# Optimization experiments

Measured on AMD Instinct MI355X. Metric: run time of the kernel, lower is better.

## Reference

```python
import jax, jax.numpy as jnp
import numpy as np

B, C, H, W = 32, 384, 32, 32
NCH = 4           # chunks per branch (mixing_size = [4,4,4])
CH = C // NCH     # 96 channels per chunk


def setup_inputs() -> dict:
    key = jax.random.key(0)
    ks = iter(jax.random.split(key, 32))
    r = lambda shape, s=0.05: jax.random.normal(next(ks), shape, dtype=jnp.float32) * s
    inp = {"x": jax.random.normal(next(ks), (B, C, H, W), dtype=jnp.float32)}
    for b, k in zip((1, 2, 3), (1, 3, 5)):
        inp[f"f{b}_mlp_w1"] = r((2, CH, CH // 8))
        inp[f"f{b}_mlp_b1"] = r((2, CH // 8))
        inp[f"f{b}_mlp_w2"] = r((2, CH // 8, CH))
        inp[f"f{b}_mlp_b2"] = r((2, CH))
        inp[f"f{b}_conv_w"] = r((2, CH, 1, k, k))
        inp[f"f{b}_conv_b"] = r((2, CH))
    inp["fusion_w1"] = r((C, C // 4))
    inp["fusion_b1"] = r((C // 4,))
    inp["fusion_w2"] = r((C // 4, 3 * C))
    inp["fusion_b2"] = r((3 * C,))
    inp["proj_w"] = r((C, C))
    inp["proj_b"] = r((C,))
    return inp


def _gelu(x):
    return jax.nn.gelu(x, approximate=False)  # torch nn.GELU default (erf)


def _branch(x, mw1, mb1, mw2, mb2, cw, cb, pad):
    # x: (B, C, H, W); chunks of CH channels; even idx -> MLP (channel-last), odd -> depthwise conv
    chunks = jnp.split(x, NCH, axis=1)
    outs, mi, ci = [], 0, 0
    for i, c in enumerate(chunks):
        if i % 2 == 0:
            h = _gelu(jnp.einsum('bchw,cd->bdhw', c, mw1[mi]) + mb1[mi][:, None, None])
            y = jnp.einsum('bdhw,dc->bchw', h, mw2[mi]) + mb2[mi][:, None, None]
            mi += 1
        else:
            y = jax.lax.conv_general_dilated(
                c, cw[ci], window_strides=(1, 1), padding=[(pad, pad), (pad, pad)],
                feature_group_count=CH, dimension_numbers=('NCHW', 'OIHW', 'NCHW'))
            y = y + cb[ci][:, None, None]
            ci += 1
        outs.append(y)
    return jnp.concatenate(outs, axis=1)


def reference(x,
              f1_mlp_w1, f1_mlp_b1, f1_mlp_w2, f1_mlp_b2, f1_conv_w, f1_conv_b,
              f2_mlp_w1, f2_mlp_b1, f2_mlp_w2, f2_mlp_b2, f2_conv_w, f2_conv_b,
              f3_mlp_w1, f3_mlp_b1, f3_mlp_w2, f3_mlp_b2, f3_conv_w, f3_conv_b,
              fusion_w1, fusion_b1, fusion_w2, fusion_b2, proj_w, proj_b):
    x1 = _branch(x, f1_mlp_w1, f1_mlp_b1, f1_mlp_w2, f1_mlp_b2, f1_conv_w, f1_conv_b, pad=0)
    x2 = _branch(x, f2_mlp_w1, f2_mlp_b1, f2_mlp_w2, f2_mlp_b2, f2_conv_w, f2_conv_b, pad=1)
    x3 = _branch(x, f3_mlp_w1, f3_mlp_b1, f3_mlp_w2, f3_mlp_b2, f3_conv_w, f3_conv_b, pad=2)
    # softmax-gated multi-scale fusion
    a = (x1 + x2 + x3).mean(axis=(2, 3))                            # (B, C)
    g = _gelu(a @ fusion_w1 + fusion_b1) @ fusion_w2 + fusion_b2     # (B, 3C)
    g = g.reshape(a.shape[0], C, 3).transpose(2, 0, 1)               # (3, B, C)
    w = jax.nn.softmax(g, axis=0)[:, :, :, None, None]               # (3, B, C, 1, 1)
    comb = x1 * w[0] + x2 * w[1] + x3 * w[2]                         # (B, C, H, W)
    out = jnp.einsum('bchw,cd->bdhw', comb, proj_w) + proj_b[:, None, None]
    return out
```

## Files before the change

### kernel.cpp

```cpp
#include <hip/hip_runtime.h>
#include <math.h>

#define B_  32
#define C_  384
#define HW  1024

typedef float          f32x4 __attribute__((ext_vector_type(4)));
typedef short          s16x8 __attribute__((ext_vector_type(8)));
typedef unsigned short us8v  __attribute__((ext_vector_type(8)));

#define SWZ(pix) ((((pix) ^ ((pix) >> 4)) & 15) << 4)

struct KParams {
  const float* x;
  const float* mw1[3]; const float* mb1[3]; const float* mw2[3]; const float* mb2[3];
  const float* cw[3];  const float* cb[3];
  const float* fw1; const float* fb1; const float* fw2; const float* fb2;
  const float* pw;  const float* pb;
  float* wg;
  float* H_part;
  float* cvA;
  float* ext;
  unsigned short* pwT;
  float* out;
};

__device__ __forceinline__ float gelu_exact(float v) {
  return 0.5f * v * (1.0f + erff(v * 0.70710678118654752440f));
}
__device__ __forceinline__ unsigned short f2bf(float f) {
  unsigned u = __float_as_uint(f);
  u += 0x7FFFu + ((u >> 16) & 1u);
  return (unsigned short)(u >> 16);
}
__device__ __forceinline__ float bf2f(unsigned short h) {
  return __uint_as_float(((unsigned)h) << 16);
}

template<int HALF>
__device__ __forceinline__ void conv_strip(const float* xc, int h0, int row,
                                           float w1t, const float* w3, const float* w5,
                                           float* y0, float* y1, float* y2) {
#pragma unroll
  for (int p = 0; p < 16; ++p) { y0[p] = 0.f; y1[p] = 0.f; y2[p] = 0.f; }
#pragma unroll
  for (int dy = 0; dy < 5; ++dy) {
    const int hr = h0 + row - 2 + dy;
    float win[20];
    if (hr >= 0 && hr < 32) {
#pragma unroll
      for (int u = 0; u < 5; ++u)
        *(float4*)&win[u*4] = *(const float4*)&xc[hr*32 + HALF*12 + u*4];
    } else {
#pragma unroll
      for (int u = 0; u < 20; ++u) win[u] = 0.f;
    }
#pragma unroll
    for (int dx = 0; dx < 5; ++dx) {
      const float w = w5[dy*5 + dx];
#pragma unroll
      for (int p = 0; p < 16; ++p) {
        const int ri = p + dx - 2 + HALF*4;
        if (ri >= 0 && ri < 20) y2[p] += win[ri] * w;
      }
    }
    if (dy >= 1 && dy <= 3) {
#pragma unroll
      for (int dx = 0; dx < 3; ++dx) {
        const float w = w3[(dy-1)*3 + dx];
#pragma unroll
        for (int p = 0; p < 16; ++p) {
          const int ri = p + dx - 1 + HALF*4;
          if (ri >= 0 && ri < 20) y1[p] += win[ri] * w;
        }
      }
      if (dy == 2) {
#pragma unroll
        for (int p = 0; p < 16; ++p) y0[p] = win[p + HALF*4] * w1t;
      }
    }
  }
}

__global__ __launch_bounds__(256, 2) void k_work(KParams P) {
  __shared__ __align__(16) char sm[49152 + 13824 + 256];
  const int bid = blockIdx.x;
  const int t = threadIdx.x;

  if (bid >= 1024) {
    const int pbk = bid - 1024;
    float (*tile)[33] = (float(*)[33])sm;
    const int td = pbk % 12, tc = pbk / 12;
    const int j = t & 31, i0 = t >> 5;
    const int gcoff = (tc < 3) ? 0 : (tc < 6 ? 96 : (tc < 9 ? -96 : 0));
    for (int i = i0; i < 32; i += 8)
      tile[i][j] = P.pw[(size_t)(tc*32 + i + gcoff)*C_ + td*32 + j];
    __syncthreads();
    for (int i = i0; i < 32; i += 8)
      P.pwT[(size_t)(td*32 + i)*C_ + tc*32 + j] = f2bf(tile[j][i]);
    return;
  }

  const int b = bid >> 5, sub = bid & 31;
  if (sub < 16) {
    const int mi = sub >> 3, q = sub & 7;
    const int h0 = q * 4;
    float* Xl  = (float*)sm;
    float* w1l = (float*)(sm + 49152);
    float* Hl  = (float*)(sm + 49152 + 13824);
    for (int i = t; i < 3456; i += 256) {
      int s = i / 1152, r = i - s*1152;
      w1l[i] = P.mw1[s][mi*1152 + r];
    }
    for (int i = t*4; i < 12288; i += 1024) {
      int c = i >> 7, pix = i & 127;
      *(float4*)&Xl[i] = *(const float4*)&P.x[(size_t)(b*C_ + mi*192 + c)*HW + h0*32 + pix];
    }
    __syncthreads();
    const int quad = t & 31, sjg = t >> 6;
    const int cq = (t >> 5) & 1;
    const int sj0 = sjg * 9;
    float h[9][4];
#pragma unroll
    for (int u = 0; u < 9; ++u) { h[u][0]=0.f; h[u][1]=0.f; h[u][2]=0.f; h[u][3]=0.f; }
    int wbase[9];
#pragma unroll
    for (int u = 0; u < 9; ++u) {
      int sj = sj0 + u, s = sj / 12, jj = sj % 12;
      wbase[u] = s*1152 + jj;
    }
    for (int c = cq*48; c < cq*48 + 48; ++c) {
      const float4 xv = *(const float4*)&Xl[c*128 + quad*4];
#pragma unroll
      for (int u = 0; u < 9; ++u) {
        const float w = w1l[wbase[u] + c*12];
        h[u][0] += xv.x*w; h[u][1] += xv.y*w; h[u][2] += xv.z*w; h[u][3] += xv.w*w;
      }
    }
#pragma unroll
    for (int u = 0; u < 9; ++u)
#pragma unroll
      for (int p = 0; p < 4; ++p) h[u][p] += __shfl_xor(h[u][p], 32, 64);
    float hs[9];
#pragma unroll
    for (int u = 0; u < 9; ++u) {
      int sj = sj0 + u, s = sj / 12, jj = sj % 12;
      const float bias = P.mb1[s][mi*12 + jj];
      float sum = 0.f;
#pragma unroll
      for (int p = 0; p < 4; ++p) sum += gelu_exact(h[u][p] + bias);
#pragma unroll
      for (int m = 16; m >= 1; m >>= 1) sum += __shfl_xor(sum, m, 64);
      hs[u] = sum;
    }
    if ((t & 63) == 0) {
#pragma unroll
      for (int u = 0; u < 9; ++u) Hl[sj0 + u] = hs[u];
    }
    __syncthreads();
    if (t < 36) P.H_part[(size_t)((b*2 + mi)*8 + q)*36 + t] = Hl[t];
  } else {
    const int s2 = sub - 16;
    const int gi = s2 >> 3, q = s2 & 7;
    const int h0 = q * 4;
    const int lane = t & 63, wv = t >> 6;
    const int gcbase = (2*gi + 1) * 96;
    for (int i = 0; i < 24; ++i) {
      const int cc = wv*24 + i;
      const float* xc = P.x + (size_t)(b*C_ + gcbase + cc)*HW + h0*32;
      const float2 v = *(const float2*)(xc + 2*lane);
      const float t2 = v.x + v.y;
      float T = t2;
      T += __shfl_xor(T, 1, 64);  T += __shfl_xor(T, 2, 64);
      T += __shfl_xor(T, 4, 64);  T += __shfl_xor(T, 8, 64);
      T += __shfl_xor(T, 16, 64); T += __shfl_xor(T, 32, 64);
      float c0  = ((lane & 15) == 0)  ? v.x : 0.f;
      float c1  = ((lane & 15) == 0)  ? v.y : 0.f;
      float c30 = ((lane & 15) == 15) ? v.x : 0.f;
      float c31 = ((lane & 15) == 15) ? v.y : 0.f;
      c0  += __shfl_xor(c0, 16, 64);  c0  += __shfl_xor(c0, 32, 64);
      c1  += __shfl_xor(c1, 16, 64);  c1  += __shfl_xor(c1, 32, 64);
      c30 += __shfl_xor(c30, 16, 64); c30 += __shfl_xor(c30, 32, 64);
      c31 += __shfl_xor(c31, 16, 64); c31 += __shfl_xor(c31, 32, 64);
      if (lane == 0) {
        float* A = &P.cvA[(size_t)(b*2 + gi)*5*96 + cc];
        atomicAdd(A + 0*96, T);   atomicAdd(A + 1*96, c0);
        atomicAdd(A + 2*96, c1);  atomicAdd(A + 3*96, c30);
        atomicAdd(A + 4*96, c31);
      }
      if (q == 0 || q == 7) {
        float r = t2;
        r += __shfl_xor(r, 1, 64); r += __shfl_xor(r, 2, 64);
        r += __shfl_xor(r, 4, 64); r += __shfl_xor(r, 8, 64);
        const int e  = (q == 0) ? 0 : 1;
        const int lo = (q == 0) ? 0 : 32;
        const float Ra  = __shfl(r,   lo,      64), Rb  = __shfl(r,   lo + 16, 64);
        const float p00 = __shfl(v.x, lo,      64), p01 = __shfl(v.y, lo,      64);
        const float p0a = __shfl(v.x, lo + 15, 64), p0b = __shfl(v.y, lo + 15, 64);
        const float p10 = __shfl(v.x, lo + 16, 64), p11 = __shfl(v.y, lo + 16, 64);
        const float p1a = __shfl(v.x, lo + 31, 64), p1b = __shfl(v.y, lo + 31, 64);
        if (lane == 0) {
          float* E = &P.ext[((size_t)(b*2 + gi)*2 + e)*10*96 + cc];
          E[0*96] = Ra;  E[1*96] = Rb;
          E[2*96] = p00; E[3*96] = p01; E[4*96] = p0a; E[5*96] = p0b;
          E[6*96] = p10; E[7*96] = p11; E[8*96] = p1a; E[9*96] = p1b;
        }
      }
    }
  }
}

__global__ __launch_bounds__(512) void k_gate(KParams P) {
  const int b = blockIdx.x, t = threadIdx.x;
  __shared__ float am[C_], g1p[4][96], g1v[96], Hs[2][36];
  for (int i = t; i < 72; i += 512) {
    int mi = i / 36, sj = i % 36;
    float s = 0.f;
    for (int q = 0; q < 8; ++q) s += P.H_part[(size_t)((b*2+mi)*8 + q)*36 + sj];
    Hs[mi][sj] = s * (1.0f/1024.0f);
  }
  __syncthreads();
  if (t < 192) {
    const int mi = t / 96, cc = t % 96;
    float a = 0.f;
    for (int s = 0; s < 3; ++s) {
      float y = P.mb2[s][mi*96 + cc];
      for (int jj = 0; jj < 12; ++jj) y += Hs[mi][s*12+jj] * P.mw2[s][mi*1152 + jj*96 + cc];
      a += y;
    }
    am[mi*192 + cc] = a;
  } else if (t < 384) {
    const int i = t - 192;
    const int gi = i / 96, cc = i % 96;
    const float* A  = &P.cvA[(size_t)(b*2 + gi)*5*96 + cc];
    const float T   = A[0*96];
    const float C0  = A[1*96], C1  = A[2*96], C30 = A[3*96], C31 = A[4*96];
    const float* E0 = &P.ext[((size_t)(b*2 + gi)*2 + 0)*10*96 + cc];
    const float* E1 = &P.ext[((size_t)(b*2 + gi)*2 + 1)*10*96 + cc];
    const float R0  = E0[0*96], R1  = E0[1*96];
    const float a00 = E0[2*96], a01 = E0[3*96], a0a = E0[4*96], a0b = E0[5*96];
    const float a10 = E0[6*96], a11 = E0[7*96], a1a = E0[8*96], a1b = E0[9*96];
    const float R30 = E1[0*96], R31 = E1[1*96];
    const float b00 = E1[2*96], b01 = E1[3*96], b0a = E1[4*96], b0b = E1[5*96];
    const float b10 = E1[6*96], b11 = E1[7*96], b1a = E1[8*96], b1b = E1[9*96];
    const float ER[5]   = {R30+R31, R31, 0.f, R0, R0+R1};
    const float EC[5]   = {C30+C31, C31, 0.f, C0, C0+C1};
    const float cr0[5]  = {a0a+a0b, a0b, 0.f, a00, a00+a01};
    const float cr1[5]  = {a1a+a1b, a1b, 0.f, a10, a10+a11};
    const float cr30[5] = {b0a+b0b, b0b, 0.f, b00, b00+b01};
    const float cr31[5] = {b1a+b1b, b1b, 0.f, b10, b10+b11};
    const int gcl = gi*96 + cc;
    float sum = P.cw[0][gcl] * T;
#pragma unroll
    for (int dy = 0; dy < 3; ++dy)
#pragma unroll
      for (int dx = 0; dx < 3; ++dx) {
        const int s = dy - 1, u = dx - 1;
        float xc_ = 0.f;
        if (s == 1)  xc_ = cr0[u+2];
        if (s == -1) xc_ = cr31[u+2];
        sum += P.cw[1][gcl*9 + dy*3 + dx] * (T - ER[s+2] - EC[u+2] + xc_);
      }
#pragma unroll
    for (int dy = 0; dy < 5; ++dy)
#pragma unroll
      for (int dx = 0; dx < 5; ++dx) {
        const int s = dy - 2, u = dx - 2;
        float xc_ = 0.f;
        if (s == 1)  xc_ = cr0[u+2];
        if (s == 2)  xc_ = cr0[u+2] + cr1[u+2];
        if (s == -1) xc_ = cr31[u+2];
        if (s == -2) xc_ = cr30[u+2] + cr31[u+2];
        sum += P.cw[2][gcl*25 + dy*5 + dx] * (T - ER[s+2] - EC[u+2] + xc_);
      }
    am[(2*gi+1)*96 + cc] = sum * (1.0f/1024.0f)
                         + P.cb[0][gcl] + P.cb[1][gcl] + P.cb[2][gcl];
  }
  __syncthreads();
  if (t < 384) {
    const int quarter = t / 96, jj = t % 96;
    float acc = 0.f;
    for (int c = quarter*96; c < quarter*96 + 96; ++c) acc += am[c] * P.fw1[c*96 + jj];
    g1p[quarter][jj] = acc;
  }
  __syncthreads();
  if (t < 96) g1v[t] = gelu_exact(g1p[0][t] + g1p[1][t] + g1p[2][t] + g1p[3][t] + P.fb1[t]);
  __syncthreads();
  if (t < 384) {
    const int c = t;
    float l0 = P.fb2[c*3+0], l1 = P.fb2[c*3+1], l2 = P.fb2[c*3+2];
    for (int jj = 0; jj < 96; ++jj) {
      const float g = g1v[jj];
      const float* f = P.fw2 + jj*1152 + c*3;
      l0 += g*f[0]; l1 += g*f[1]; l2 += g*f[2];
    }
    const float m = fmaxf(l0, fmaxf(l1, l2));
    const float e0 = expf(l0-m), e1 = expf(l1-m), e2 = expf(l2-m);
    const float inv = 1.0f/(e0+e1+e2);
    P.wg[0*(B_*C_) + b*C_ + c] = e0*inv;
    P.wg[1*(B_*C_) + b*C_ + c] = e1*inv;
    P.wg[2*(B_*C_) + b*C_ + c] = e2*inv;
  }
}

template<int HALF>
__device__ __forceinline__ void conv_phase2(const KParams& P, int b, int h0,
                                            char* combB, const float* wgl, int tt) {
  for (int it = 0; it < 2; ++it) {
    const int task = tt + 512*it;
    if (task < 768) {
      const int row = task & 3, c192 = task >> 2;
      const int gi = c192 / 96, cc = c192 - gi*96;
      const int gcl = gi*96 + cc;
      const int gc = (2*gi + 1)*96 + cc;
      const int kp = 192 + gi*96 + cc;
      const float* xc = P.x + (size_t)(b*C_ + gc)*HW;
      const float w1t = P.cw[0][gcl];
      float w3[9], w5[25];
#pragma unroll
      for (int k2 = 0; k2 < 9; ++k2)  w3[k2] = P.cw[1][gcl*9 + k2];
#pragma unroll
      for (int k2 = 0; k2 < 25; ++k2) w5[k2] = P.cw[2][gcl*25 + k2];
      float y0[16], y1[16], y2[16];
      conv_strip<HALF>(xc, h0, row, w1t, w3, w5, y0, y1, y2);
      const float g0 = wgl[0*C_ + gc], g1 = wgl[1*C_ + gc], g2 = wgl[2*C_ + gc];
      const float cbg = g0*P.cb[0][gcl] + g1*P.cb[1][gcl] + g2*P.cb[2][gcl];
#pragma unroll
      for (int p = 0; p < 16; ++p) {
        const float v = g0*y0[p] + g1*y1[p] + g2*y2[p] + cbg;
        const int pix = row*32 + HALF*16 + p;
        const int off = pix*768 + ((kp*2) ^ SWZ(pix));
        *(unsigned short*)(combB + off) = f2bf(v);
      }
    }
  }
}

__global__ __launch_bounds__(1024, 4) void k_proj(KParams P) {
  __shared__ __align__(16) char smem[159744];
  char* combB = smem;
  char* hlB   = smem + 98304;
  char* XB    = smem + 116736;
  unsigned short* wlB = (unsigned short*)(smem + 141312);
  float* wgl  = (float*)(smem + 155136);

  const int t  = threadIdx.x;
  const int rb = (blockIdx.x & 7) * 32 + (blockIdx.x >> 3);
  const int b  = rb >> 3;
  const int h0 = (rb & 7) * 4;

  for (int i = t; i < 1152; i += 1024)
    wgl[i] = P.wg[(size_t)(i/C_)*(B_*C_) + b*C_ + (i % C_)];
  for (int i = t; i < 6912; i += 1024) {
    int s = i / 2304, r = i - s*2304, mi2 = r / 1152, rr = r - mi2*1152;
    int c = rr / 12, jj = rr - c*12;
    wlB[(s*2 + mi2)*1152 + jj*96 + c] = f2bf(P.mw1[s][mi2*1152 + rr]);
  }
  for (int i = t*4; i < 12288; i += 4096) {
    int c = i >> 7, pix = i & 127;
    float4 v = *(const float4*)&P.x[(size_t)(b*C_ + c)*HW + h0*32 + pix];
    unsigned lo = (unsigned)f2bf(v.x) | ((unsigned)f2bf(v.y) << 16);
    unsigned hi = (unsigned)f2bf(v.z) | ((unsigned)f2bf(v.w) << 16);
    *(uint2*)(XB + c*256 + pix*2) = make_uint2(lo, hi);
  }
  __syncthreads();

#pragma unroll 1
  for (int mi = 0; mi < 2; ++mi) {
    if (t < 512) {
      const int w = t >> 6, l = t & 63;
      const int nsj = (w < 4) ? 5 : 4;
      const int sj0 = (w < 4) ? w*5 : 20 + (w - 4)*4;
      int wbase[5]; float bias[5];
#pragma unroll
      for (int u = 0; u < 5; ++u) {
        int sj = sj0 + ((u < nsj) ? u : 0);
        int s = sj / 12, jj = sj - s*12;
        wbase[u] = (s*2 + mi)*1152 + jj*96;
        bias[u] = P.mb1[s][mi*12 + jj];
      }
      float h[5][2];
#pragma unroll
      for (int u = 0; u < 5; ++u) { h[u][0] = 0.f; h[u][1] = 0.f; }
      for (int c0 = 0; c0 < 96; c0 += 8) {
        us8v wv8[5];
#pragma unroll
        for (int u = 0; u < 5; ++u)
          wv8[u] = *(const us8v*)(wlB + wbase[u] + c0);
#pragma unroll
        for (int cc = 0; cc < 8; ++cc) {
          const unsigned xp = *(const unsigned*)(XB + (c0 + cc)*256 + l*4);
          const float x0 = __uint_as_float(xp << 16);
          const float x1 = __uint_as_float(xp & 0xFFFF0000u);
#pragma unroll
          for (int u = 0; u < 5; ++u) {
            if (u < nsj) {
              const float wv = bf2f(wv8[u][cc]);
              h[u][0] += x0*wv; h[u][1] += x1*wv;
            }
          }
        }
      }
#pragma unroll
      for (int u = 0; u < 5; ++u) {
        if (u < nsj) {
          const unsigned o = (unsigned)f2bf(gelu_exact(h[u][0] + bias[u]))
                           | ((unsigned)f2bf(gelu_exact(h[u][1] + bias[u])) << 16);
          *(unsigned*)(hlB + (mi*36 + sj0 + u)*256 + l*4) = o;
        }
      }
    } else {
      if (mi == 0) conv_phase2<0>(P, b, h0, combB, wgl, t - 512);
      else         conv_phase2<1>(P, b, h0, combB, wgl, t - 512);
    }
    __syncthreads();
    if (mi == 0) {
      for (int i = t*4; i < 12288; i += 4096) {
        int c = i >> 7, pix = i & 127;
        float4 v = *(const float4*)&P.x[(size_t)(b*C_ + 192 + c)*HW + h0*32 + pix];
        unsigned lo = (unsigned)f2bf(v.x) | ((unsigned)f2bf(v.y) << 16);
        unsigned hi = (unsigned)f2bf(v.z) | ((unsigned)f2bf(v.w) << 16);
        *(uint2*)(XB + c*256 + pix*2) = make_uint2(lo, hi);
      }
      __syncthreads();
    }
  }

  for (int i = t; i < 6912; i += 1024) {
    int s = i / 2304, r = i - s*2304, mi2 = r / 1152, rr = r - mi2*1152;
    wlB[(s*2 + mi2)*1152 + rr] = f2bf(P.mw2[s][mi2*1152 + rr]);
  }
  __syncthreads();

  {
    const int ct = t & 31, pt = (t >> 5) & 15, mi = t >> 9;
    const int c0 = ct*3, pix0 = pt*8;
    float wgc[3][3];
#pragma unroll
    for (int s = 0; s < 3; ++s)
#pragma unroll
      for (int i = 0; i < 3; ++i) wgc[s][i] = wgl[s*C_ + mi*192 + c0 + i];
    float acc[3][8];
#pragma unroll
    for (int i = 0; i < 3; ++i) {
      float ai = 0.f;
#pragma unroll
      for (int s = 0; s < 3; ++s) ai += wgc[s][i] * P.mb2[s][mi*96 + c0 + i];
#pragma unroll
      for (int p = 0; p < 8; ++p) acc[i][p] = ai;
    }
#pragma unroll
    for (int s = 0; s < 3; ++s)
#pragma unroll
      for (int jj = 0; jj < 12; ++jj) {
        const us8v hv = *(const us8v*)(hlB + (mi*36 + s*12 + jj)*256 + pix0*2);
        float hf[8];
#pragma unroll
        for (int p = 0; p < 8; ++p) hf[p] = bf2f(hv[p]);
        const unsigned short* wp = wlB + (s*2 + mi)*1152 + jj*96 + c0;
        float gw[3];
#pragma unroll
        for (int i = 0; i < 3; ++i) gw[i] = bf2f(wp[i]) * wgc[s][i];
#pragma unroll
        for (int i = 0; i < 3; ++i)
#pragma unroll
          for (int p = 0; p < 8; ++p) acc[i][p] += gw[i]*hf[p];
      }
#pragma unroll
    for (int i = 0; i < 3; ++i)
#pragma unroll
      for (int p = 0; p < 8; ++p) {
        const int pix = pix0 + p;
        const int kp2 = mi*96 + c0 + i;
        const int off = pix*768 + ((kp2*2) ^ SWZ(pix));
        *(unsigned short*)(combB + off) = f2bf(acc[i][p]);
      }
  }
  __syncthreads();

  {
    const int lane = t & 63, wv = t >> 6;
    const int wm = wv & 1, wn = wv >> 1;
    const int l15 = lane & 15, l4 = lane >> 4;
    f32x4 acc[4][3];
#pragma unroll
    for (int mt = 0; mt < 4; ++mt)
#pragma unroll
      for (int nt = 0; nt < 3; ++nt) acc[mt][nt] = (f32x4){0.f,0.f,0.f,0.f};
    const char* pwTb = (const char*)P.pwT;
#pragma unroll 2
    for (int ks = 0; ks < 12; ++ks) {
      const int k0 = ks*32 + l4*8;
      s16x8 af[4], bfr[3];
#pragma unroll
      for (int mt = 0; mt < 4; ++mt) {
        const int m = wm*64 + mt*16 + l15;
        af[mt] = *(const s16x8*)(combB + m*768 + ((2*k0) ^ SWZ(m)));
      }
#pragma unroll
      for (int nt = 0; nt < 3; ++nt) {
        const int d = wn*48 + nt*16 + l15;
        bfr[nt] = *(const s16x8*)(pwTb + (size_t)d*768 + 2*k0);
      }
#pragma unroll
      for (int mt = 0; mt < 4; ++mt)
#pragma unroll
        for (int nt = 0; nt < 3; ++nt)
          acc[mt][nt] = __builtin_amdgcn_mfma_f32_16x16x32_bf16(af[mt], bfr[nt], acc[mt][nt], 0, 0, 0);
    }
#pragma unroll
    for (int nt = 0; nt < 3; ++nt) {
      const int d = wn*48 + nt*16 + l15;
      const float pbv = P.pb[d];
#pragma unroll
      for (int mt = 0; mt < 4; ++mt) {
        const int pix = wm*64 + mt*16 + l4*4;
        float4 o;
        o.x = acc[mt][nt][0] + pbv;
        o.y = acc[mt][nt][1] + pbv;
        o.z = acc[mt][nt][2] + pbv;
        o.w = acc[mt][nt][3] + pbv;
        *(float4*)&P.out[(size_t)(b*C_ + d)*HW + (h0 + (pix >> 5))*32 + (pix & 31)] = o;
      }
    }
  }
}

extern "C" void kernel_launch(void* const* d_in, const int* in_sizes, int n_in,
                              void* d_out, int out_size, void* d_ws, size_t ws_size,
                              hipStream_t stream) {
  KParams P;
  P.x = (const float*)d_in[0];
  for (int s = 0; s < 3; ++s) {
    const int base = 1 + s * 6;
    P.mw1[s] = (const float*)d_in[base + 0];
    P.mb1[s] = (const float*)d_in[base + 1];
    P.mw2[s] = (const float*)d_in[base + 2];
    P.mb2[s] = (const float*)d_in[base + 3];
    P.cw[s]  = (const float*)d_in[base + 4];
    P.cb[s]  = (const float*)d_in[base + 5];
  }
  P.fw1 = (const float*)d_in[19]; P.fb1 = (const float*)d_in[20];
  P.fw2 = (const float*)d_in[21]; P.fb2 = (const float*)d_in[22];
  P.pw  = (const float*)d_in[23]; P.pb  = (const float*)d_in[24];
  float* w = (float*)d_ws;
  P.wg     = w;
  P.H_part = w + 36864;
  P.cvA    = w + 55296;
  P.ext    = w + 86016;
  P.pwT    = (unsigned short*)(w + 208896);
  P.out = (float*)d_out;

  hipMemsetAsync((char*)d_ws + 55296*sizeof(float), 0, 30720*sizeof(float), stream);
  k_work<<<1168, 256, 0, stream>>>(P);
  k_gate<<<32, 512, 0, stream>>>(P);
  k_proj<<<256, 1024, 0, stream>>>(P);
}
```

Before: 289.8 us.

## Store MLP hidden activations in k_work and reuse them in k_proj

The first kernel now writes the GELU hidden activations as bf16 to a workspace buffer. The projection kernel reads them back instead of recomputing the first MLP layer, which removes the x reload and the hidden-layer recompute from k_proj. Conv partial sums are now written per strip and summed in the gate kernel rather than accumulated with atomics, so the memset can be dropped. k_proj shrinks to 512 threads with more channels per thread. The trade-off is extra global write and read traffic for the hidden buffer and lower thread-level parallelism in k_proj.

```diff
diff --git a/kernel.cpp b/kernel.cpp
--- a/kernel.cpp
+++ b/kernel.cpp
@@ -19,9 +19,10 @@
   const float* pw;  const float* pb;
   float* wg;
   float* H_part;
-  float* cvA;
+  float* cvS;
   float* ext;
   unsigned short* pwT;
+  unsigned short* hl;
   float* out;
 };
 
@@ -146,9 +147,16 @@
     for (int u = 0; u < 9; ++u) {
       int sj = sj0 + u, s = sj / 12, jj = sj % 12;
       const float bias = P.mb1[s][mi*12 + jj];
-      float sum = 0.f;
-#pragma unroll
-      for (int p = 0; p < 4; ++p) sum += gelu_exact(h[u][p] + bias);
+      float g[4];
+#pragma unroll
+      for (int p = 0; p < 4; ++p) g[p] = gelu_exact(h[u][p] + bias);
+      if ((t & 63) < 32) {
+        uint2 pk;
+        pk.x = (unsigned)f2bf(g[0]) | ((unsigned)f2bf(g[1]) << 16);
+        pk.y = (unsigned)f2bf(g[2]) | ((unsigned)f2bf(g[3]) << 16);
+        *(uint2*)(P.hl + ((size_t)(b*2 + mi)*36 + sj)*1024 + q*128 + quad*4) = pk;
+      }
+      float sum = g[0] + g[1] + g[2] + g[3];
 #pragma unroll
       for (int m = 16; m >= 1; m >>= 1) sum += __shfl_xor(sum, m, 64);
       hs[u] = sum;
@@ -183,10 +191,9 @@
       c30 += __shfl_xor(c30, 16, 64); c30 += __shfl_xor(c30, 32, 64);
       c31 += __shfl_xor(c31, 16, 64); c31 += __shfl_xor(c31, 32, 64);
       if (lane == 0) {
-        float* A = &P.cvA[(size_t)(b*2 + gi)*5*96 + cc];
-        atomicAdd(A + 0*96, T);   atomicAdd(A + 1*96, c0);
-        atomicAdd(A + 2*96, c1);  atomicAdd(A + 3*96, c30);
-        atomicAdd(A + 4*96, c31);
+        float* S = &P.cvS[(((size_t)(b*2 + gi)*8 + q)*5)*96 + cc];
+        S[0*96] = T;   S[1*96] = c0;  S[2*96] = c1;
+        S[3*96] = c30; S[4*96] = c31;
       }
       if (q == 0 || q == 7) {
         float r = t2;
@@ -232,9 +239,13 @@
   } else if (t < 384) {
     const int i = t - 192;
     const int gi = i / 96, cc = i % 96;
-    const float* A  = &P.cvA[(size_t)(b*2 + gi)*5*96 + cc];
-    const float T   = A[0*96];
-    const float C0  = A[1*96], C1  = A[2*96], C30 = A[3*96], C31 = A[4*96];
+    const float* S0 = &P.cvS[(((size_t)(b*2 + gi)*8)*5)*96 + cc];
+    float T = 0.f, C0 = 0.f, C1 = 0.f, C30 = 0.f, C31 = 0.f;
+#pragma unroll
+    for (int q = 0; q < 8; ++q) {
+      const float* Sq = S0 + (size_t)q*5*96;
+      T += Sq[0*96]; C0 += Sq[1*96]; C1 += Sq[2*96]; C30 += Sq[3*96]; C31 += Sq[4*96];
+    }
     const float* E0 = &P.ext[((size_t)(b*2 + gi)*2 + 0)*10*96 + cc];
     const float* E1 = &P.ext[((size_t)(b*2 + gi)*2 + 1)*10*96 + cc];
     const float R0  = E0[0*96], R1  = E0[1*96];
@@ -303,146 +314,73 @@
   }
 }
 
-template<int HALF>
-__device__ __forceinline__ void conv_phase2(const KParams& P, int b, int h0,
-                                            char* combB, const float* wgl, int tt) {
-  for (int it = 0; it < 2; ++it) {
-    const int task = tt + 512*it;
-    if (task < 768) {
-      const int row = task & 3, c192 = task >> 2;
-      const int gi = c192 / 96, cc = c192 - gi*96;
-      const int gcl = gi*96 + cc;
-      const int gc = (2*gi + 1)*96 + cc;
-      const int kp = 192 + gi*96 + cc;
-      const float* xc = P.x + (size_t)(b*C_ + gc)*HW;
-      const float w1t = P.cw[0][gcl];
-      float w3[9], w5[25];
-#pragma unroll
-      for (int k2 = 0; k2 < 9; ++k2)  w3[k2] = P.cw[1][gcl*9 + k2];
-#pragma unroll
-      for (int k2 = 0; k2 < 25; ++k2) w5[k2] = P.cw[2][gcl*25 + k2];
-      float y0[16], y1[16], y2[16];
-      conv_strip<HALF>(xc, h0, row, w1t, w3, w5, y0, y1, y2);
-      const float g0 = wgl[0*C_ + gc], g1 = wgl[1*C_ + gc], g2 = wgl[2*C_ + gc];
-      const float cbg = g0*P.cb[0][gcl] + g1*P.cb[1][gcl] + g2*P.cb[2][gcl];
-#pragma unroll
-      for (int p = 0; p < 16; ++p) {
-        const float v = g0*y0[p] + g1*y1[p] + g2*y2[p] + cbg;
-        const int pix = row*32 + HALF*16 + p;
-        const int off = pix*768 + ((kp*2) ^ SWZ(pix));
-        *(unsigned short*)(combB + off) = f2bf(v);
-      }
-    }
-  }
-}
-
-__global__ __launch_bounds__(1024, 4) void k_proj(KParams P) {
-  __shared__ __align__(16) char smem[159744];
+__global__ __launch_bounds__(512, 1) void k_proj(KParams P) {
+  __shared__ __align__(16) char smem[135168];
   char* combB = smem;
   char* hlB   = smem + 98304;
-  char* XB    = smem + 116736;
-  unsigned short* wlB = (unsigned short*)(smem + 141312);
-  float* wgl  = (float*)(smem + 155136);
+  unsigned short* wlB = (unsigned short*)(smem + 117120);
+  float* wgl  = (float*)(smem + 130944);
 
   const int t  = threadIdx.x;
   const int rb = (blockIdx.x & 7) * 32 + (blockIdx.x >> 3);
   const int b  = rb >> 3;
-  const int h0 = (rb & 7) * 4;
-
-  for (int i = t; i < 1152; i += 1024)
+  const int qv = rb & 7;
+  const int h0 = qv * 4;
+
+  for (int i = t; i < 1152; i += 512)
     wgl[i] = P.wg[(size_t)(i/C_)*(B_*C_) + b*C_ + (i % C_)];
-  for (int i = t; i < 6912; i += 1024) {
-    int s = i / 2304, r = i - s*2304, mi2 = r / 1152, rr = r - mi2*1152;
-    int c = rr / 12, jj = rr - c*12;
-    wlB[(s*2 + mi2)*1152 + jj*96 + c] = f2bf(P.mw1[s][mi2*1152 + rr]);
-  }
-  for (int i = t*4; i < 12288; i += 4096) {
-    int c = i >> 7, pix = i & 127;
-    float4 v = *(const float4*)&P.x[(size_t)(b*C_ + c)*HW + h0*32 + pix];
-    unsigned lo = (unsigned)f2bf(v.x) | ((unsigned)f2bf(v.y) << 16);
-    unsigned hi = (unsigned)f2bf(v.z) | ((unsigned)f2bf(v.w) << 16);
-    *(uint2*)(XB + c*256 + pix*2) = make_uint2(lo, hi);
-  }
-  __syncthreads();
-
-#pragma unroll 1
-  for (int mi = 0; mi < 2; ++mi) {
-    if (t < 512) {
-      const int w = t >> 6, l = t & 63;
-      const int nsj = (w < 4) ? 5 : 4;
-      const int sj0 = (w < 4) ? w*5 : 20 + (w - 4)*4;
-      int wbase[5]; float bias[5];
-#pragma unroll
-      for (int u = 0; u < 5; ++u) {
-        int sj = sj0 + ((u < nsj) ? u : 0);
-        int s = sj / 12, jj = sj - s*12;
-        wbase[u] = (s*2 + mi)*1152 + jj*96;
-        bias[u] = P.mb1[s][mi*12 + jj];
-      }
-      float h[5][2];
-#pragma unroll
-      for (int u = 0; u < 5; ++u) { h[u][0] = 0.f; h[u][1] = 0.f; }
-      for (int c0 = 0; c0 < 96; c0 += 8) {
-        us8v wv8[5];
-#pragma unroll
-        for (int u = 0; u < 5; ++u)
-          wv8[u] = *(const us8v*)(wlB + wbase[u] + c0);
-#pragma unroll
-        for (int cc = 0; cc < 8; ++cc) {
-          const unsigned xp = *(const unsigned*)(XB + (c0 + cc)*256 + l*4);
-          const float x0 = __uint_as_float(xp << 16);
-          const float x1 = __uint_as_float(xp & 0xFFFF0000u);
-#pragma unroll
-          for (int u = 0; u < 5; ++u) {
-            if (u < nsj) {
-              const float wv = bf2f(wv8[u][cc]);
-              h[u][0] += x0*wv; h[u][1] += x1*wv;
-            }
-          }
-        }
-      }
-#pragma unroll
-      for (int u = 0; u < 5; ++u) {
-        if (u < nsj) {
-          const unsigned o = (unsigned)f2bf(gelu_exact(h[u][0] + bias[u]))
-                           | ((unsigned)f2bf(gelu_exact(h[u][1] + bias[u])) << 16);
-          *(unsigned*)(hlB + (mi*36 + sj0 + u)*256 + l*4) = o;
-        }
-      }
-    } else {
-      if (mi == 0) conv_phase2<0>(P, b, h0, combB, wgl, t - 512);
-      else         conv_phase2<1>(P, b, h0, combB, wgl, t - 512);
-    }
-    __syncthreads();
-    if (mi == 0) {
-      for (int i = t*4; i < 12288; i += 4096) {
-        int c = i >> 7, pix = i & 127;
-        float4 v = *(const float4*)&P.x[(size_t)(b*C_ + 192 + c)*HW + h0*32 + pix];
-        unsigned lo = (unsigned)f2bf(v.x) | ((unsigned)f2bf(v.y) << 16);
-        unsigned hi = (unsigned)f2bf(v.z) | ((unsigned)f2bf(v.w) << 16);
-        *(uint2*)(XB + c*256 + pix*2) = make_uint2(lo, hi);
-      }
-      __syncthreads();
-    }
-  }
-
-  for (int i = t; i < 6912; i += 1024) {
-    int s = i / 2304, r = i - s*2304, mi2 = r / 1152, rr = r - mi2*1152;
-    wlB[(s*2 + mi2)*1152 + rr] = f2bf(P.mw2[s][mi2*1152 + rr]);
-  }
-  __syncthreads();
+  for (int i = t; i < 6912; i += 512) {
+    int s = i / 2304, r = i - s*2304;
+    wlB[i] = f2bf(P.mw2[s][r]);
+  }
+  for (int i = t; i < 2304; i += 512) {
+    const int sjmi = i >> 5, pg = i & 31;
+    const uint2 v = *(const uint2*)(P.hl + ((size_t)(b*72 + sjmi))*1024 + qv*128 + pg*4);
+    *(uint2*)(hlB + sjmi*256 + pg*8) = v;
+  }
+  __syncthreads();
+
+  for (int it = 0; it < 3; ++it) {
+    const int tt = t + 512*it;
+    const int hlf = (tt >= 768) ? 1 : 0;
+    const int rem = tt - hlf*768;
+    const int row = rem & 3, c192 = rem >> 2;
+    const int gi = c192 / 96, cc = c192 - gi*96;
+    const int gcl = gi*96 + cc;
+    const int gc = (2*gi + 1)*96 + cc;
+    const int kp = 192 + gi*96 + cc;
+    const float* xc = P.x + (size_t)(b*C_ + gc)*HW;
+    const float w1t = P.cw[0][gcl];
+    float w3[9], w5[25];
+#pragma unroll
+    for (int k2 = 0; k2 < 9; ++k2)  w3[k2] = P.cw[1][gcl*9 + k2];
+#pragma unroll
+    for (int k2 = 0; k2 < 25; ++k2) w5[k2] = P.cw[2][gcl*25 + k2];
+    float y0[16], y1[16], y2[16];
+    if (hlf == 0) conv_strip<0>(xc, h0, row, w1t, w3, w5, y0, y1, y2);
+    else          conv_strip<1>(xc, h0, row, w1t, w3, w5, y0, y1, y2);
+    const float g0 = wgl[0*C_ + gc], g1 = wgl[1*C_ + gc], g2 = wgl[2*C_ + gc];
+    const float cbg = g0*P.cb[0][gcl] + g1*P.cb[1][gcl] + g2*P.cb[2][gcl];
+#pragma unroll
+    for (int p = 0; p < 16; ++p) {
+      const float v = g0*y0[p] + g1*y1[p] + g2*y2[p] + cbg;
+      const int pix = row*32 + hlf*16 + p;
+      const int off = pix*768 + ((kp*2) ^ SWZ(pix));
+      *(unsigned short*)(combB + off) = f2bf(v);
+    }
+  }
 
   {
-    const int ct = t & 31, pt = (t >> 5) & 15, mi = t >> 9;
-    const int c0 = ct*3, pix0 = pt*8;
-    float wgc[3][3];
+    const int ct = t & 15, pt = (t >> 4) & 15, mi = t >> 8;
+    const int c0 = ct*6, pix0 = pt*8;
+    float wgc[3][6];
 #pragma unroll
     for (int s = 0; s < 3; ++s)
 #pragma unroll
-      for (int i = 0; i < 3; ++i) wgc[s][i] = wgl[s*C_ + mi*192 + c0 + i];
-    float acc[3][8];
-#pragma unroll
-    for (int i = 0; i < 3; ++i) {
+      for (int i = 0; i < 6; ++i) wgc[s][i] = wgl[s*C_ + mi*192 + c0 + i];
+    float acc[6][8];
+#pragma unroll
+    for (int i = 0; i < 6; ++i) {
       float ai = 0.f;
 #pragma unroll
       for (int s = 0; s < 3; ++s) ai += wgc[s][i] * P.mb2[s][mi*96 + c0 + i];
@@ -458,16 +396,16 @@
 #pragma unroll
         for (int p = 0; p < 8; ++p) hf[p] = bf2f(hv[p]);
         const unsigned short* wp = wlB + (s*2 + mi)*1152 + jj*96 + c0;
-        float gw[3];
-#pragma unroll
-        for (int i = 0; i < 3; ++i) gw[i] = bf2f(wp[i]) * wgc[s][i];
-#pragma unroll
-        for (int i = 0; i < 3; ++i)
+        float gw[6];
+#pragma unroll
+        for (int i = 0; i < 6; ++i) gw[i] = bf2f(wp[i]) * wgc[s][i];
+#pragma unroll
+        for (int i = 0; i < 6; ++i)
 #pragma unroll
           for (int p = 0; p < 8; ++p) acc[i][p] += gw[i]*hf[p];
       }
 #pragma unroll
-    for (int i = 0; i < 3; ++i)
+    for (int i = 0; i < 6; ++i)
 #pragma unroll
       for (int p = 0; p < 8; ++p) {
         const int pix = pix0 + p;
@@ -482,35 +420,35 @@
     const int lane = t & 63, wv = t >> 6;
     const int wm = wv & 1, wn = wv >> 1;
     const int l15 = lane & 15, l4 = lane >> 4;
-    f32x4 acc[4][3];
+    f32x4 acc[4][6];
 #pragma unroll
     for (int mt = 0; mt < 4; ++mt)
 #pragma unroll
-      for (int nt = 0; nt < 3; ++nt) acc[mt][nt] = (f32x4){0.f,0.f,0.f,0.f};
+      for (int nt = 0; nt < 6; ++nt) acc[mt][nt] = (f32x4){0.f,0.f,0.f,0.f};
     const char* pwTb = (const char*)P.pwT;
 #pragma unroll 2
     for (int ks = 0; ks < 12; ++ks) {
       const int k0 = ks*32 + l4*8;
-      s16x8 af[4], bfr[3];
+      s16x8 af[4], bfr[6];
 #pragma unroll
       for (int mt = 0; mt < 4; ++mt) {
         const int m = wm*64 + mt*16 + l15;
         af[mt] = *(const s16x8*)(combB + m*768 + ((2*k0) ^ SWZ(m)));
       }
 #pragma unroll
-      for (int nt = 0; nt < 3; ++nt) {
-        const int d = wn*48 + nt*16 + l15;
+      for (int nt = 0; nt < 6; ++nt) {
+        const int d = wn*96 + nt*16 + l15;
         bfr[nt] = *(const s16x8*)(pwTb + (size_t)d*768 + 2*k0);
       }
 #pragma unroll
       for (int mt = 0; mt < 4; ++mt)
 #pragma unroll
-        for (int nt = 0; nt < 3; ++nt)
+        for (int nt = 0; nt < 6; ++nt)
           acc[mt][nt] = __builtin_amdgcn_mfma_f32_16x16x32_bf16(af[mt], bfr[nt], acc[mt][nt], 0, 0, 0);
     }
 #pragma unroll
-    for (int nt = 0; nt < 3; ++nt) {
-      const int d = wn*48 + nt*16 + l15;
+    for (int nt = 0; nt < 6; ++nt) {
+      const int d = wn*96 + nt*16 + l15;
       const float pbv = P.pb[d];
 #pragma unroll
       for (int mt = 0; mt < 4; ++mt) {
@@ -546,13 +484,13 @@
   float* w = (float*)d_ws;
   P.wg     = w;
   P.H_part = w + 36864;
-  P.cvA    = w + 55296;
-  P.ext    = w + 86016;
-  P.pwT    = (unsigned short*)(w + 208896);
+  P.cvS    = w + 55296;
+  P.ext    = w + 301056;
+  P.pwT    = (unsigned short*)(w + 423936);
+  P.hl     = (unsigned short*)(w + 497664);
   P.out = (float*)d_out;
 
-  hipMemsetAsync((char*)d_ws + 55296*sizeof(float), 0, 30720*sizeof(float), stream);
   k_work<<<1168, 256, 0, stream>>>(P);
   k_gate<<<32, 512, 0, stream>>>(P);
-  k_proj<<<256, 1024, 0, stream>>>(P);
-}
+  k_proj<<<256, 512, 0, stream>>>(P);
+}
```

New measurement: 248.2 us. -14.3%, faster.
